# Kernel optimization log

Measured on AMD Instinct MI355X. Metric: run time of the kernel, lower is better.

## Reference

```python
import jax, jax.numpy as jnp
import numpy as np

B, S, D = 64, 1024, 256
N_HEADS = 1
HEAD_DIM = D // N_HEADS
MASK_VAL = -10000.0


def setup_inputs() -> dict:
    key = jax.random.key(0)
    k1, k2, k3 = jax.random.split(key, 3)
    x = jax.random.normal(k1, (B, S, D), dtype=jnp.float32)
    W_qkv = jax.random.normal(k2, (D, 3 * D), dtype=jnp.float32) * 0.02
    b_qkv = jnp.zeros((3 * D,), dtype=jnp.float32)
    W_out = jax.random.normal(k3, (D, D), dtype=jnp.float32) * 0.02
    b_out = jnp.zeros((D,), dtype=jnp.float32)
    return {"x": x, "W_qkv": W_qkv, "b_qkv": b_qkv, "W_out": W_out, "b_out": b_out}


def reference(x, W_qkv, b_qkv, W_out, b_out):
    # QKV projection: [B,S,3D]
    qkv = jnp.einsum('bsd,df->bsf', x, W_qkv) + b_qkv
    q, k, v = jnp.split(qkv, 3, axis=2)
    # split heads -> [B,H,S,hd] (H=1)
    def split_heads(t):
        return t.reshape(B, S, N_HEADS, HEAD_DIM).transpose(0, 2, 1, 3)
    q, k, v = split_heads(q), split_heads(k), split_heads(v)
    # scaled scores [B,H,S,S]
    scores = jnp.einsum('bhqd,bhkd->bhqk', q, k) / jnp.sqrt(jnp.float32(HEAD_DIM))
    causal = jnp.tril(jnp.ones((1, 1, S, S), dtype=bool))
    scores = jnp.where(causal, scores, jnp.float32(MASK_VAL))
    attn = jax.nn.softmax(scores, axis=-1)  # dropout deterministic (training=False)
    out = jnp.einsum('bhqk,bhkd->bhqd', attn, v)
    # merge heads -> [B,S,D]
    out = out.transpose(0, 2, 1, 3).reshape(B, S, D)
    out = jnp.einsum('bsd,de->bse', out, W_out) + b_out
    return out, attn
```

## Files before the change

kernel.cpp:

```cpp
#include <hip/hip_runtime.h>
#include <hip/hip_bf16.h>

#define BB 64
#define SS 1024
#define DDIM 256

typedef unsigned short u16;
typedef unsigned int u32;
typedef __attribute__((ext_vector_type(4))) float f4;
typedef __attribute__((ext_vector_type(8))) short bf16x8;
typedef __attribute__((ext_vector_type(4))) short bf16x4;
typedef __attribute__((ext_vector_type(4))) float f32x4;

__device__ inline u16 f2b(float f) {
  unsigned int u = __float_as_uint(f);
  unsigned int r = (u + 0x7fffu + ((u >> 16) & 1u)) >> 16;
  return (u16)r;
}
__device__ inline float b2f(u16 v) {
  return __uint_as_float(((u32)v) << 16);
}

__global__ __launch_bounds__(256) void cast_x(const float* __restrict__ x,
                                              u16* __restrict__ xb, int n8) {
  int i = blockIdx.x * 256 + threadIdx.x;
  const int stride = gridDim.x * 256;
  for (; i < n8; i += stride) {
    f4 a = ((const f4*)x)[2 * i];
    f4 b = ((const f4*)x)[2 * i + 1];
    bf16x8 o;
    o[0] = f2b(a[0]); o[1] = f2b(a[1]); o[2] = f2b(a[2]); o[3] = f2b(a[3]);
    o[4] = f2b(b[0]); o[5] = f2b(b[1]); o[6] = f2b(b[2]); o[7] = f2b(b[3]);
    ((bf16x8*)xb)[i] = o;
  }
}

__global__ __launch_bounds__(256) void cast_w(const float* __restrict__ Wqkv,
                                              const float* __restrict__ Wout,
                                              u16* __restrict__ Wqkvt,
                                              u16* __restrict__ Woutt) {
  int t = blockIdx.x * 256 + threadIdx.x;
  if (t < 256 * 768) {
    int k = t / 768, n = t % 768;
    Wqkvt[n * 256 + k] = f2b(Wqkv[t]);
  }
  if (t < 256 * 256) {
    int k = t / 256, n = t % 256;
    Woutt[n * 256 + k] = f2b(Wout[t]);
  }
}

template <int EPI, int NXT>
__global__ __launch_bounds__(512) void gemm_mfma(
    const u16* __restrict__ A, const u16* __restrict__ Bt,
    const float* __restrict__ bias, float* __restrict__ outF,
    u16* __restrict__ Qb, u16* __restrict__ Kb, u16* __restrict__ Vt) {
  __shared__ u16 As[128 * 64];
  __shared__ u16 Bs[256 * 64];
  const int t = threadIdx.x;
  const int w = t >> 6, l = t & 63;
  const int lr = l & 15, lg = l >> 4;
  const int id = blockIdx.x;
  const int r8 = id & 7;
  const int tt = id >> 3;
  const int xt = tt % NXT;
  const int yt = (tt / NXT) * 8 + r8;
  const int m0 = yt * 128, n0 = xt * 256;
  const int wm = (w >> 2) * 64, wn = (w & 3) * 64;

  f32x4 acc[4][4] = {};

  for (int k0 = 0; k0 < 256; k0 += 64) {
    __syncthreads();
#pragma unroll
    for (int j = 0; j < 2; ++j) {
      const int idx = t + j * 512;
      const int row = idx >> 3, c = idx & 7;
      f4 va = *(const f4*)&A[(size_t)(m0 + row) * 256 + k0 + c * 8];
      *(f4*)&As[row * 64 + ((c ^ (row & 7)) * 8)] = va;
    }
#pragma unroll
    for (int j = 0; j < 4; ++j) {
      const int idx = t + j * 512;
      const int row = idx >> 3, c = idx & 7;
      f4 vb = *(const f4*)&Bt[(size_t)(n0 + row) * 256 + k0 + c * 8];
      *(f4*)&Bs[row * 64 + ((c ^ (row & 7)) * 8)] = vb;
    }
    __syncthreads();
#pragma unroll
    for (int kc = 0; kc < 2; ++kc) {
      bf16x8 af[4], bfr[4];
#pragma unroll
      for (int f = 0; f < 4; ++f) {
        int ar = wm + f * 16 + lr;
        af[f] = *(const bf16x8*)&As[ar * 64 + (((kc * 4 + lg) ^ (ar & 7)) * 8)];
        int br = wn + f * 16 + lr;
        bfr[f] = *(const bf16x8*)&Bs[br * 64 + (((kc * 4 + lg) ^ (br & 7)) * 8)];
      }
#pragma unroll
      for (int i = 0; i < 4; ++i)
#pragma unroll
        for (int jn = 0; jn < 4; ++jn)
          acc[i][jn] = __builtin_amdgcn_mfma_f32_16x16x32_bf16(
              af[i], bfr[jn], acc[i][jn], 0, 0, 0);
    }
  }

#pragma unroll
  for (int i = 0; i < 4; ++i) {
    const int mbase = m0 + wm + i * 16 + lg * 4;
#pragma unroll
    for (int jn = 0; jn < 4; ++jn) {
      const int n = n0 + wn + jn * 16 + lr;
      const float bv = bias[n];
      if (EPI == 0) {
#pragma unroll
        for (int r = 0; r < 4; ++r)
          outF[(size_t)(mbase + r) * 256 + n] = acc[i][jn][r] + bv;
      } else {
        if (n < 256) {
#pragma unroll
          for (int r = 0; r < 4; ++r)
            Qb[(size_t)(mbase + r) * 256 + n] = f2b(acc[i][jn][r] + bv);
        } else if (n < 512) {
#pragma unroll
          for (int r = 0; r < 4; ++r)
            Kb[(size_t)(mbase + r) * 256 + (n - 256)] = f2b(acc[i][jn][r] + bv);
        } else {
          const int d = n - 512;
          const int b = mbase >> 10, sl = mbase & 1023;
          bf16x4 pk;
#pragma unroll
          for (int r = 0; r < 4; ++r) pk[r] = f2b(acc[i][jn][r] + bv);
          *(bf16x4*)&Vt[((size_t)b * 256 + d) * 1024 + sl] = pk;
        }
      }
    }
  }
}

__global__ __launch_bounds__(256) void attn_fused(
    const u16* __restrict__ Qg, const u16* __restrict__ Kg,
    const u16* __restrict__ Vtg, float* __restrict__ attn,
    u16* __restrict__ outa) {
  __shared__ u16 pool[40960];
  u16* P = pool;
  u16* Ks = pool + 32768;
  float* rsF = (float*)(pool + 32768);

  const int t = threadIdx.x;
  const int w = t >> 6, l = t & 63;
  const int lr = l & 15, lg = l >> 4;
  const int id = blockIdx.x;
  const int b = 8 * (id & 7) + ((id >> 3) & 7);
  const int zb = id >> 6;
  const int qt = 15 - (zb >> 1);
  const int h = 1 - (zb & 1);
  const int qrow0 = qt * 64 + h * 32;
  const int last = 2 * qt + h;
  const int qh = w & 1, sfh = w >> 1;
  const int d0 = w * 64;

  const u16* Kbase = Kg + (size_t)b * SS * DDIM;
  const u16* Vbase = Vtg + (size_t)b * DDIM * SS;

  bf16x8 qf[8];
  {
    const u16* qp = Qg + ((size_t)(b * SS + qrow0 + qh * 16 + lr)) * DDIM;
#pragma unroll
    for (int kc = 0; kc < 8; ++kc)
      qf[kc] = *(const bf16x8*)&qp[kc * 32 + lg * 8];
  }

  {
    f4 kreg[4];
#pragma unroll
    for (int j = 0; j < 4; ++j) {
      const int cid = t + j * 256;
      const int row = cid >> 5, ch = cid & 31;
      kreg[j] = *(const f4*)&Kbase[(size_t)row * 256 + ch * 8];
#pragma unroll
      for (int jj = 0; jj <= 0; ++jj) {
        const int sw = (ch & 24) | ((ch & 7) ^ (row & 7));
        *(f4*)&Ks[row * 256 + sw * 8] = kreg[j];
      }
    }
  }
  __syncthreads();

  bf16x8 vfr[4];
#pragma unroll
  for (int df = 0; df < 4; ++df)
    vfr[df] = *(const bf16x8*)&Vbase[(size_t)(d0 + df * 16 + lr) * SS + lg * 8];

  float ra[4] = {0.f, 0.f, 0.f, 0.f};
  f32x4 oacc[2][4];
#pragma unroll
  for (int qb = 0; qb < 2; ++qb)
#pragma unroll
    for (int df = 0; df < 4; ++df) oacc[qb][df] = (f32x4){0.f, 0.f, 0.f, 0.f};

  for (int kt = 0; kt <= last; ++kt) {
    f4 kregN[4];
    bf16x8 vfrN[4];
    if (kt < last) {
#pragma unroll
      for (int j = 0; j < 4; ++j) {
        const int cid = t + j * 256;
        const int row = cid >> 5, ch = cid & 31;
        kregN[j] =
            *(const f4*)&Kbase[(size_t)((kt + 1) * 32 + row) * 256 + ch * 8];
      }
#pragma unroll
      for (int df = 0; df < 4; ++df)
        vfrN[df] = *(const bf16x8*)&Vbase[(size_t)(d0 + df * 16 + lr) * SS +
                                          (kt + 1) * 32 + lg * 8];
    }
    {
      const int srow = sfh * 16 + lr;
      f32x4 s = {0.f, 0.f, 0.f, 0.f};
#pragma unroll
      for (int kc = 0; kc < 8; ++kc) {
        const int c = kc * 4 + lg;
        const int ch = (c & 24) | ((c & 7) ^ (srow & 7));
        bf16x8 bfr = *(const bf16x8*)&Ks[srow * 256 + ch * 8];
        s = __builtin_amdgcn_mfma_f32_16x16x32_bf16(qf[kc], bfr, s, 0, 0, 0);
      }
      const int qmin = qrow0 + qh * 16;
      float p[4];
      if (kt * 32 + sfh * 16 + 16 <= qmin) {
#pragma unroll
        for (int r = 0; r < 4; ++r) p[r] = __expf(s[r] * 0.0625f);
      } else {
        const int scol = kt * 32 + sfh * 16 + lr;
#pragma unroll
        for (int r = 0; r < 4; ++r)
          p[r] = (scol <= qmin + lg * 4 + r) ? __expf(s[r] * 0.0625f) : 0.f;
      }
#pragma unroll
      for (int r = 0; r < 4; ++r) {
        ra[r] += p[r];
        const int row = qh * 16 + lg * 4 + r;
        const int col = kt * 32 + sfh * 16 + lr;
        const int c = col >> 3;
        const int sw = (c & ~7) | ((c & 7) ^ (row & 7));
        P[row * 1024 + sw * 8 + (col & 7)] = f2b(p[r]);
      }
    }
    __syncthreads();
    if (kt < last) {
#pragma unroll
      for (int j = 0; j < 4; ++j) {
        const int cid = t + j * 256;
        const int row = cid >> 5, ch = cid & 31;
        const int sw = (ch & 24) | ((ch & 7) ^ (row & 7));
        *(f4*)&Ks[row * 256 + sw * 8] = kregN[j];
      }
    }
#pragma unroll
    for (int qb = 0; qb < 2; ++qb) {
      const int row = qb * 16 + lr;
      const int c = kt * 4 + lg;
      const int sw = (c & ~7) | ((c & 7) ^ (row & 7));
      bf16x8 pa = *(const bf16x8*)&P[row * 1024 + sw * 8];
#pragma unroll
      for (int df = 0; df < 4; ++df)
        oacc[qb][df] = __builtin_amdgcn_mfma_f32_16x16x32_bf16(
            pa, vfr[df], oacc[qb][df], 0, 0, 0);
    }
    if (kt < last) {
#pragma unroll
      for (int df = 0; df < 4; ++df) vfr[df] = vfrN[df];
      __syncthreads();
    }
  }

#pragma unroll
  for (int m = 1; m < 16; m <<= 1)
#pragma unroll
    for (int r = 0; r < 4; ++r) ra[r] += __shfl_xor(ra[r], m, 64);
  if (lr == 0) {
#pragma unroll
    for (int r = 0; r < 4; ++r)
      rsF[sfh * 32 + qh * 16 + lg * 4 + r] = ra[r];
  }
  __syncthreads();

  {
    float* attnb = attn + ((size_t)(b * SS + qrow0)) * SS;
    const int row = w * 8 + (l >> 3);
    const float invr = 1.0f / (rsF[row] + rsF[32 + row]);
    const int kend = (last + 1) * 32;
    for (int c0 = 0; c0 < kend; c0 += 32) {
      const int col = c0 + (l & 7) * 4;
      const int c = col >> 3;
      const int sw = (c & ~7) | ((c & 7) ^ (row & 7));
      bf16x4 pv = *(const bf16x4*)&P[row * 1024 + sw * 8 + (col & 7)];
      f4 o;
#pragma unroll
      for (int j = 0; j < 4; ++j) o[j] = b2f((u16)pv[j]) * invr;
      *(f4*)&attnb[(size_t)row * SS + col] = o;
    }
    const f4 z = {0.f, 0.f, 0.f, 0.f};
    for (int c0 = kend; c0 < SS; c0 += 32)
      *(f4*)&attnb[(size_t)row * SS + c0 + (l & 7) * 4] = z;
  }
  __syncthreads();

#pragma unroll
  for (int qb = 0; qb < 2; ++qb) {
#pragma unroll
    for (int r = 0; r < 4; ++r) {
      const int row = qb * 16 + lg * 4 + r;
      const float invv = 1.0f / (rsF[row] + rsF[32 + row]);
#pragma unroll
      for (int df = 0; df < 4; ++df)
        pool[row * 264 + d0 + df * 16 + lr] = f2b(oacc[qb][df][r] * invv);
    }
  }
  __syncthreads();
  {
    const int row = t >> 3;
    const int cb = (t & 7) * 32;
    u16* og = outa + ((size_t)(b * SS + qrow0 + row)) * DDIM + cb;
#pragma unroll
    for (int k = 0; k < 4; ++k) {
      bf16x8 v = *(const bf16x8*)&pool[row * 264 + cb + k * 8];
      *(bf16x8*)&og[k * 8] = v;
    }
  }
}

extern "C" void kernel_launch(void* const* d_in, const int* in_sizes, int n_in,
                              void* d_out, int out_size, void* d_ws,
                              size_t ws_size, hipStream_t stream) {
  const float* x    = (const float*)d_in[0];
  const float* Wqkv = (const float*)d_in[1];
  const float* bqkv = (const float*)d_in[2];
  const float* Wout = (const float*)d_in[3];
  const float* bout = (const float*)d_in[4];

  float* out  = (float*)d_out;
  float* attn = out + (size_t)BB * SS * DDIM;

  const size_t NTOK = (size_t)BB * SS;
  u16* ws = (u16*)d_ws;
  u16* xb    = ws;
  u16* Qb    = xb + NTOK * DDIM;
  u16* Kb    = Qb + NTOK * DDIM;
  u16* Vt    = Kb + NTOK * DDIM;
  u16* outa  = Vt + NTOK * DDIM;
  u16* Wqkvt = outa + NTOK * DDIM;
  u16* Woutt = Wqkvt + 768 * 256;

  cast_x<<<2048, 256, 0, stream>>>(x, xb, (int)(NTOK * DDIM / 8));
  cast_w<<<768, 256, 0, stream>>>(Wqkv, Wout, Wqkvt, Woutt);

  gemm_mfma<1, 3><<<1536, 512, 0, stream>>>(xb, Wqkvt, bqkv, nullptr, Qb, Kb,
                                            Vt);
  attn_fused<<<2048, 256, 0, stream>>>(Qb, Kb, Vt, attn, outa);
  gemm_mfma<0, 1><<<512, 512, 0, stream>>>(outa, Woutt, bout, out, nullptr,
                                           nullptr, nullptr);
}
```

Before: 249.6 us.

## Fuse output projection into attention kernel and merge cast kernels

Each attention block now multiplies its normalized 32x256 output tile by W_out with MFMA, adds the bias, and writes fp32 output directly. This removes the bf16 intermediate round trip and the separate output GEMM launch. The two cast kernels are merged into one launch. The cost is extra work in the attention kernel: W_out fragments are read from global memory per block without LDS staging, and register pressure goes up.

New measurement: 247.2 us, median of 3. Within noise of the previous version (-1.0%).

```diff
diff --git a/kernel.cpp b/kernel.cpp
--- a/kernel.cpp
+++ b/kernel.cpp
@@ -21,11 +21,21 @@
   return __uint_as_float(((u32)v) << 16);
 }
 
-__global__ __launch_bounds__(256) void cast_x(const float* __restrict__ x,
-                                              u16* __restrict__ xb, int n8) {
-  int i = blockIdx.x * 256 + threadIdx.x;
+__global__ __launch_bounds__(256) void cast_all(
+    const float* __restrict__ x, const float* __restrict__ Wqkv,
+    const float* __restrict__ Wout, u16* __restrict__ xb,
+    u16* __restrict__ Wqkvt, u16* __restrict__ Woutt, int n8) {
+  const int gid = blockIdx.x * 256 + threadIdx.x;
+  if (gid < 256 * 768) {
+    int k = gid / 768, n = gid % 768;
+    Wqkvt[n * 256 + k] = f2b(Wqkv[gid]);
+  }
+  if (gid < 256 * 256) {
+    int k = gid / 256, n = gid % 256;
+    Woutt[n * 256 + k] = f2b(Wout[gid]);
+  }
   const int stride = gridDim.x * 256;
-  for (; i < n8; i += stride) {
+  for (int i = gid; i < n8; i += stride) {
     f4 a = ((const f4*)x)[2 * i];
     f4 b = ((const f4*)x)[2 * i + 1];
     bf16x8 o;
@@ -35,26 +45,11 @@
   }
 }
 
-__global__ __launch_bounds__(256) void cast_w(const float* __restrict__ Wqkv,
-                                              const float* __restrict__ Wout,
-                                              u16* __restrict__ Wqkvt,
-                                              u16* __restrict__ Woutt) {
-  int t = blockIdx.x * 256 + threadIdx.x;
-  if (t < 256 * 768) {
-    int k = t / 768, n = t % 768;
-    Wqkvt[n * 256 + k] = f2b(Wqkv[t]);
-  }
-  if (t < 256 * 256) {
-    int k = t / 256, n = t % 256;
-    Woutt[n * 256 + k] = f2b(Wout[t]);
-  }
-}
-
-template <int EPI, int NXT>
-__global__ __launch_bounds__(512) void gemm_mfma(
+template <int NXT>
+__global__ __launch_bounds__(512) void gemm_qkv(
     const u16* __restrict__ A, const u16* __restrict__ Bt,
-    const float* __restrict__ bias, float* __restrict__ outF,
-    u16* __restrict__ Qb, u16* __restrict__ Kb, u16* __restrict__ Vt) {
+    const float* __restrict__ bias, u16* __restrict__ Qb,
+    u16* __restrict__ Kb, u16* __restrict__ Vt) {
   __shared__ u16 As[128 * 64];
   __shared__ u16 Bs[256 * 64];
   const int t = threadIdx.x;
@@ -113,27 +108,21 @@
     for (int jn = 0; jn < 4; ++jn) {
       const int n = n0 + wn + jn * 16 + lr;
       const float bv = bias[n];
-      if (EPI == 0) {
+      if (n < 256) {
 #pragma unroll
         for (int r = 0; r < 4; ++r)
-          outF[(size_t)(mbase + r) * 256 + n] = acc[i][jn][r] + bv;
+          Qb[(size_t)(mbase + r) * 256 + n] = f2b(acc[i][jn][r] + bv);
+      } else if (n < 512) {
+#pragma unroll
+        for (int r = 0; r < 4; ++r)
+          Kb[(size_t)(mbase + r) * 256 + (n - 256)] = f2b(acc[i][jn][r] + bv);
       } else {
-        if (n < 256) {
-#pragma unroll
-          for (int r = 0; r < 4; ++r)
-            Qb[(size_t)(mbase + r) * 256 + n] = f2b(acc[i][jn][r] + bv);
-        } else if (n < 512) {
-#pragma unroll
-          for (int r = 0; r < 4; ++r)
-            Kb[(size_t)(mbase + r) * 256 + (n - 256)] = f2b(acc[i][jn][r] + bv);
-        } else {
-          const int d = n - 512;
-          const int b = mbase >> 10, sl = mbase & 1023;
-          bf16x4 pk;
-#pragma unroll
-          for (int r = 0; r < 4; ++r) pk[r] = f2b(acc[i][jn][r] + bv);
-          *(bf16x4*)&Vt[((size_t)b * 256 + d) * 1024 + sl] = pk;
-        }
+        const int d = n - 512;
+        const int b = mbase >> 10, sl = mbase & 1023;
+        bf16x4 pk;
+#pragma unroll
+        for (int r = 0; r < 4; ++r) pk[r] = f2b(acc[i][jn][r] + bv);
+        *(bf16x4*)&Vt[((size_t)b * 256 + d) * 1024 + sl] = pk;
       }
     }
   }
@@ -141,12 +130,14 @@
 
 __global__ __launch_bounds__(256) void attn_fused(
     const u16* __restrict__ Qg, const u16* __restrict__ Kg,
-    const u16* __restrict__ Vtg, float* __restrict__ attn,
-    u16* __restrict__ outa) {
+    const u16* __restrict__ Vtg, const u16* __restrict__ Woutt,
+    const float* __restrict__ bout, float* __restrict__ attn,
+    float* __restrict__ out) {
   __shared__ u16 pool[40960];
   u16* P = pool;
   u16* Ks = pool + 32768;
   float* rsF = (float*)(pool + 32768);
+  float* fout = (float*)pool;
 
   const int t = threadIdx.x;
   const int w = t >> 6, l = t & 63;
@@ -173,17 +164,13 @@
   }
 
   {
-    f4 kreg[4];
 #pragma unroll
     for (int j = 0; j < 4; ++j) {
       const int cid = t + j * 256;
       const int row = cid >> 5, ch = cid & 31;
-      kreg[j] = *(const f4*)&Kbase[(size_t)row * 256 + ch * 8];
-#pragma unroll
-      for (int jj = 0; jj <= 0; ++jj) {
-        const int sw = (ch & 24) | ((ch & 7) ^ (row & 7));
-        *(f4*)&Ks[row * 256 + sw * 8] = kreg[j];
-      }
+      f4 kv = *(const f4*)&Kbase[(size_t)row * 256 + ch * 8];
+      const int sw = (ch & 24) | ((ch & 7) ^ (row & 7));
+      *(f4*)&Ks[row * 256 + sw * 8] = kv;
     }
   }
   __syncthreads();
@@ -285,6 +272,15 @@
       rsF[sfh * 32 + qh * 16 + lg * 4 + r] = ra[r];
   }
   __syncthreads();
+
+  float invq[2][4];
+#pragma unroll
+  for (int qb = 0; qb < 2; ++qb)
+#pragma unroll
+    for (int r = 0; r < 4; ++r) {
+      const int row = qb * 16 + lg * 4 + r;
+      invq[qb][r] = 1.0f / (rsF[row] + rsF[32 + row]);
+    }
 
   {
     float* attnb = attn + ((size_t)(b * SS + qrow0)) * SS;
@@ -308,25 +304,65 @@
   __syncthreads();
 
 #pragma unroll
-  for (int qb = 0; qb < 2; ++qb) {
-#pragma unroll
-    for (int r = 0; r < 4; ++r) {
-      const int row = qb * 16 + lg * 4 + r;
-      const float invv = 1.0f / (rsF[row] + rsF[32 + row]);
+  for (int qb = 0; qb < 2; ++qb)
+#pragma unroll
+    for (int df = 0; df < 4; ++df)
+#pragma unroll
+      for (int r = 0; r < 4; ++r) {
+        const int row = qb * 16 + lg * 4 + r;
+        const int col = d0 + df * 16 + lr;
+        const int c = col >> 3;
+        const int sw = (c & ~7) | ((c & 7) ^ (row & 7));
+        Ks[row * 256 + sw * 8 + (col & 7)] = f2b(oacc[qb][df][r] * invq[qb][r]);
+      }
+  __syncthreads();
+
+  f32x4 wacc[2][4];
+#pragma unroll
+  for (int qb = 0; qb < 2; ++qb)
+#pragma unroll
+    for (int df = 0; df < 4; ++df) wacc[qb][df] = (f32x4){0.f, 0.f, 0.f, 0.f};
+#pragma unroll
+  for (int kc = 0; kc < 8; ++kc) {
+    bf16x8 af[2], bfr[4];
+#pragma unroll
+    for (int qb = 0; qb < 2; ++qb) {
+      const int row = qb * 16 + lr;
+      const int c = kc * 4 + lg;
+      const int sw = (c & ~7) | ((c & 7) ^ (row & 7));
+      af[qb] = *(const bf16x8*)&Ks[row * 256 + sw * 8];
+    }
+#pragma unroll
+    for (int df = 0; df < 4; ++df)
+      bfr[df] = *(const bf16x8*)&Woutt[(size_t)(d0 + df * 16 + lr) * 256 +
+                                       kc * 32 + lg * 8];
+#pragma unroll
+    for (int qb = 0; qb < 2; ++qb)
 #pragma unroll
       for (int df = 0; df < 4; ++df)
-        pool[row * 264 + d0 + df * 16 + lr] = f2b(oacc[qb][df][r] * invv);
-    }
-  }
-  __syncthreads();
+        wacc[qb][df] = __builtin_amdgcn_mfma_f32_16x16x32_bf16(
+            af[qb], bfr[df], wacc[qb][df], 0, 0, 0);
+  }
+#pragma unroll
+  for (int df = 0; df < 4; ++df) {
+    const int n = d0 + df * 16 + lr;
+    const float bv = bout[n];
+#pragma unroll
+    for (int qb = 0; qb < 2; ++qb)
+#pragma unroll
+      for (int r = 0; r < 4; ++r)
+        fout[(qb * 16 + lg * 4 + r) * 260 + n] = wacc[qb][df][r] + bv;
+  }
+  __syncthreads();
+
   {
     const int row = t >> 3;
     const int cb = (t & 7) * 32;
-    u16* og = outa + ((size_t)(b * SS + qrow0 + row)) * DDIM + cb;
-#pragma unroll
-    for (int k = 0; k < 4; ++k) {
-      bf16x8 v = *(const bf16x8*)&pool[row * 264 + cb + k * 8];
-      *(bf16x8*)&og[k * 8] = v;
+    float* og = out + ((size_t)(b * SS + qrow0 + row)) * DDIM + cb;
+#pragma unroll
+    for (int k = 0; k < 8; ++k) {
+      f4 v = *(const f4*)&fout[row * 260 + cb + k * 4];
+      *(f4*)&og[k * 4] = v;
     }
   }
 }
@@ -349,16 +385,11 @@
   u16* Qb    = xb + NTOK * DDIM;
   u16* Kb    = Qb + NTOK * DDIM;
   u16* Vt    = Kb + NTOK * DDIM;
-  u16* outa  = Vt + NTOK * DDIM;
-  u16* Wqkvt = outa + NTOK * DDIM;
+  u16* Wqkvt = Vt + NTOK * DDIM;
   u16* Woutt = Wqkvt + 768 * 256;
 
-  cast_x<<<2048, 256, 0, stream>>>(x, xb, (int)(NTOK * DDIM / 8));
-  cast_w<<<768, 256, 0, stream>>>(Wqkv, Wout, Wqkvt, Woutt);
-
-  gemm_mfma<1, 3><<<1536, 512, 0, stream>>>(xb, Wqkvt, bqkv, nullptr, Qb, Kb,
-                                            Vt);
-  attn_fused<<<2048, 256, 0, stream>>>(Qb, Kb, Vt, attn, outa);
-  gemm_mfma<0, 1><<<512, 512, 0, stream>>>(outa, Woutt, bout, out, nullptr,
-                                           nullptr, nullptr);
-}
+  cast_all<<<2048, 256, 0, stream>>>(x, Wqkv, Wout, xb, Wqkvt, Woutt,
+                                     (int)(NTOK * DDIM / 8));
+  gemm_qkv<3><<<1536, 512, 0, stream>>>(xb, Wqkvt, bqkv, Qb, Kb, Vt);
+  attn_fused<<<2048, 256, 0, stream>>>(Qb, Kb, Vt, Woutt, bout, attn, out);
+}
```
